# Performance work log

Hardware: AMD Instinct MI355X
Metric: run time of the kernel (lower is better)

The kernel has to match this reference:

```python
import jax, jax.numpy as jnp
import numpy as np

EPS = 1e-10

def setup_inputs() -> dict:
    key = jax.random.key(0)
    ks = jax.random.split(key, 7)
    B, S, C, H, W = 8, 4, 512, 64, 64
    Cq = C // 4
    x = jax.random.normal(ks[0], (B, S, C, H, W), dtype=jnp.float32)
    wq = jax.random.normal(ks[1], (S, Cq, C), dtype=jnp.float32) * 0.02
    bq = jax.random.normal(ks[2], (S, Cq), dtype=jnp.float32) * 0.02
    wk = jax.random.normal(ks[3], (S, Cq, C), dtype=jnp.float32) * 0.02
    bk = jax.random.normal(ks[4], (S, Cq), dtype=jnp.float32) * 0.02
    wv = jax.random.normal(ks[5], (S, C, C), dtype=jnp.float32) * 0.02
    bv = jax.random.normal(ks[6], (S, C), dtype=jnp.float32) * 0.02
    gamma = jnp.zeros((1,), dtype=jnp.float32)
    return {"x": x, "wq": wq, "bq": bq, "wk": wk, "bk": bk,
            "wv": wv, "bv": bv, "gamma": gamma}

def reference(x, wq, bq, wk, bk, wv, bv, gamma):
    # x: (B, S, C, H, W); per-scale 1x1 convs == per-pixel matmuls
    B, S, C, H, W = x.shape
    q = jnp.einsum('bschw,soc->bsohw', x, wq) + bq[None, :, :, None, None]
    k = jnp.einsum('bschw,soc->bsohw', x, wk) + bk[None, :, :, None, None]
    v = jnp.einsum('bschw,soc->bsohw', x, wv) + bv[None, :, :, None, None]
    pq = q.reshape(B, S, -1)                      # (B, S, D)
    pk = k.reshape(B, S, -1).transpose(0, 2, 1)   # (B, D, S)
    pv = v.reshape(B, S, -1)                      # (B, S, C*H*W)
    # L2 normalization (cosine similarity), matching torch eps placement
    A1 = pq / (jnp.sqrt(jnp.sum(pq * pq, axis=-1, keepdims=True)) + EPS)
    B1 = pk / (jnp.sqrt(jnp.sum(pk * pk, axis=1, keepdims=True)) + EPS)
    energy = jnp.einsum('bsd,bdt->bst', A1, B1)   # (B, S, S)
    attention = jax.nn.softmax(energy, axis=-1)
    out = jnp.einsum('bst,btd->bsd', attention, pv).reshape(B, S, C, H, W)
    out = gamma[0] * out + x
    # original returns list [out[:, i]] for i in range(S); return stacked tensor
    return out
```

## Files before the change

kernel.cpp:

```cpp
#include <hip/hip_runtime.h>
#include <hip/hip_bf16.h>

#define EPS_F 1e-10f

typedef short s16x8 __attribute__((ext_vector_type(8)));
typedef float f32x4 __attribute__((ext_vector_type(4)));
typedef unsigned short ushort_t;

constexpr int B_ = 8, S_ = 4, C_ = 512, Cq_ = 128, HW_ = 4096;
constexpr long long D_ = (long long)Cq_ * HW_;

__device__ inline float bf_lo(unsigned int u) { return __uint_as_float(u << 16); }
__device__ inline float bf_hi(unsigned int u) { return __uint_as_float(u & 0xffff0000u); }

__device__ inline ushort_t f2bf(float f) {
    __hip_bfloat16 h = __float2bfloat16(f);
    return *reinterpret_cast<ushort_t*>(&h);
}
__device__ inline unsigned int pack_bf2(float a, float b) {
    return (unsigned int)f2bf(a) | ((unsigned int)f2bf(b) << 16);
}
__device__ inline float dot8(uint4 a, uint4 b) {
    return bf_lo(a.x) * bf_lo(b.x) + bf_hi(a.x) * bf_hi(b.x)
         + bf_lo(a.y) * bf_lo(b.y) + bf_hi(a.y) * bf_hi(b.y)
         + bf_lo(a.z) * bf_lo(b.z) + bf_hi(a.z) * bf_hi(b.z)
         + bf_lo(a.w) * bf_lo(b.w) + bf_hi(a.w) * bf_hi(b.w);
}

#define GLOAD16(gp, lp) __builtin_amdgcn_global_load_lds( \
    (const __attribute__((address_space(1))) unsigned int*)(gp), \
    (__attribute__((address_space(3))) unsigned int*)(lp), 16, 0, 0)

#define VMCNT0 asm volatile("s_waitcnt vmcnt(0)" ::: "memory")
#define LGK0   asm volatile("s_waitcnt lgkmcnt(0)" ::: "memory")
#define MFMA16(a, b, c) __builtin_amdgcn_mfma_f32_16x16x32_bf16(a, b, c, 0, 0, 0)

#define SWZ(p) ((((p) >> 3) & 7) ^ ((p) & 7))

__global__ __launch_bounds__(256) void prep3(
    const float* __restrict__ wq, const float* __restrict__ wk,
    const float* __restrict__ wv,
    ushort_t* __restrict__ Wqk_pre, ushort_t* __restrict__ Wvb_pre,
    float* __restrict__ g4) {
    int gid = blockIdx.x * 256 + threadIdx.x;
    if (gid < 8 * 24 * 16) g4[gid] = 0.f;
    if (gid < 65536) {
        int s = gid >> 14;
        int kt = (gid >> 11) & 7;
        int row = (gid >> 3) & 255;
        int slot = gid & 7;
        int col = kt * 64 + ((slot ^ (row & 7)) << 3);
        const float* src = (row < 128)
            ? &wq[((size_t)s * 128 + row) * 512 + col]
            : &wk[((size_t)s * 128 + (row - 128)) * 512 + col];
        float4 f0 = *reinterpret_cast<const float4*>(src);
        float4 f1 = *reinterpret_cast<const float4*>(src + 4);
        uint4 o;
        o.x = pack_bf2(f0.x, f0.y); o.y = pack_bf2(f0.z, f0.w);
        o.z = pack_bf2(f1.x, f1.y); o.w = pack_bf2(f1.z, f1.w);
        *reinterpret_cast<uint4*>(Wqk_pre + (size_t)gid * 8) = o;
    } else {
        int c2 = gid - 65536;
        int t = c2 >> 15;
        int ct = (c2 >> 14) & 1;
        int kt = (c2 >> 11) & 7;
        int row = (c2 >> 3) & 255;
        int slot = c2 & 7;
        int col = kt * 64 + ((slot ^ (row & 7)) << 3);
        const float* src = &wv[((size_t)t * 512 + ct * 256 + row) * 512 + col];
        float4 f0 = *reinterpret_cast<const float4*>(src);
        float4 f1 = *reinterpret_cast<const float4*>(src + 4);
        uint4 o;
        o.x = pack_bf2(f0.x, f0.y); o.y = pack_bf2(f0.z, f0.w);
        o.z = pack_bf2(f1.x, f1.y); o.w = pack_bf2(f1.z, f1.w);
        *reinterpret_cast<uint4*>(Wvb_pre + (size_t)c2 * 8) = o;
    }
}

__global__ __launch_bounds__(512, 8) void qk8(
    const ushort_t* __restrict__ Wqk_pre, const float* __restrict__ x,
    const float* __restrict__ bq, const float* __restrict__ bk,
    ushort_t* __restrict__ Qb, ushort_t* __restrict__ Kb,
    ushort_t* __restrict__ xbfT) {

    const int xcd = blockIdx.x & 7;
    const int idx = blockIdx.x >> 3;
    const int bt = xcd * 4 + (idx >> 8);
    const int s = bt & 3;
    const int pb = (idx >> 1) & 127;
    const int ob = idx & 1;
    const int p0 = pb * 32;

    __shared__ __align__(16) ushort_t AsAll[2 * 8192];
    __shared__ __align__(16) ushort_t BsAll[2 * 2048];

    const int tid = threadIdx.x;
    const int w = tid >> 6, lane = tid & 63;
    const int wr = w >> 1, wc = w & 1;
    const int li = lane & 15, lk = lane >> 4;
    const int arow = wr * 32;
    const int bp = wc * 16 + li;
    int a_sl[2], b_sl[2];
#pragma unroll
    for (int h = 0; h < 2; ++h) {
        a_sl[h] = (((h * 4 + lk) ^ (li & 7)) << 3);
        b_sl[h] = (((h * 4 + lk) ^ SWZ(bp)) << 3);
    }

    const int sk = tid >> 3, spb = (tid & 7) * 4;
    const int ep = tid >> 3, esl = tid & 7;
    const int ec = esl ^ SWZ(ep);

    const float* Bx = x + (size_t)bt * C_ * HW_ + p0 + spb;

    f32x4 acc[2];
    acc[0] = 0.f; acc[1] = 0.f;
    float4 nb;

#define STAGE_A8(T, BUF)                                                     \
    { const ushort_t* _tp = Wqk_pre + ((size_t)(s * 8 + (T)) << 14)          \
                            + (ob << 13);                                    \
      ushort_t* _ld = &AsAll[(BUF) * 8192];                                  \
      _Pragma("unroll")                                                      \
      for (int _i = 0; _i < 2; ++_i)                                         \
          GLOAD16(_tp + ((w * 2 + _i) << 9) + (lane << 3),                   \
                  _ld + ((w * 2 + _i) << 9)); }

#define LOAD_B8(T) nb = *reinterpret_cast<const float4*>(Bx + (size_t)((T) * 64 + sk) * HW_)

#define WRITE_B8(BUF)                                                        \
    { float _vv[4] = {nb.x, nb.y, nb.z, nb.w};                               \
      _Pragma("unroll")                                                      \
      for (int _j = 0; _j < 4; ++_j) {                                       \
          int _p = spb + _j;                                                 \
          BsAll[(BUF) * 2048 + _p * 64 + (((sk >> 3) ^ SWZ(_p)) << 3)        \
                + (sk & 7)] = f2bf(_vv[_j]);                                 \
      } }

#define EMIT8(T, BUF)                                                        \
    if (ob == 0 && w < 4) {                                                  \
        s16x8 _ev = *reinterpret_cast<const s16x8*>(&BsAll[(BUF) * 2048 + tid * 8]); \
        *reinterpret_cast<s16x8*>(                                           \
            xbfT + ((size_t)bt * HW_ + p0 + ep) * 512 + (T) * 64 + ec * 8) = _ev; \
    }

#define COMPUTE8(BUF)                                                        \
    { const int _ab = (BUF) * 8192, _bb = (BUF) * 2048;                      \
      _Pragma("unroll")                                                      \
      for (int h = 0; h < 2; ++h) {                                          \
          s16x8 af0 = *reinterpret_cast<const s16x8*>(                       \
              &AsAll[_ab + (arow + 0 * 16 + li) * 64 + a_sl[h]]);            \
          s16x8 af1 = *reinterpret_cast<const s16x8*>(                       \
              &AsAll[_ab + (arow + 1 * 16 + li) * 64 + a_sl[h]]);            \
          s16x8 bf = *reinterpret_cast<const s16x8*>(                        \
              &BsAll[_bb + bp * 64 + b_sl[h]]);                              \
          __builtin_amdgcn_s_setprio(1);                                     \
          acc[0] = MFMA16(af0, bf, acc[0]);                                  \
          acc[1] = MFMA16(af1, bf, acc[1]);                                  \
          __builtin_amdgcn_s_setprio(0);                                     \
      } }

    LOAD_B8(0);
    STAGE_A8(0, 0);
    WRITE_B8(0);
    VMCNT0; LGK0;
    __builtin_amdgcn_s_barrier();

#pragma unroll
    for (int t = 0; t < 8; ++t) {
        if (t < 7) { LOAD_B8(t + 1); STAGE_A8(t + 1, (t + 1) & 1); }
        EMIT8(t, t & 1);
        COMPUTE8(t & 1);
        if (t < 7) {
            WRITE_B8((t + 1) & 1);
            VMCNT0; LGK0;
            __builtin_amdgcn_s_barrier();
        }
    }

#undef STAGE_A8
#undef LOAD_B8
#undef WRITE_B8
#undef EMIT8
#undef COMPUTE8

    ushort_t* outp = ob ? Kb : Qb;
    const float* biasp = ob ? (bk + s * 128) : (bq + s * 128);
#pragma unroll
    for (int mf = 0; mf < 2; ++mf) {
#pragma unroll
        for (int r = 0; r < 4; ++r) {
            int m = arow + mf * 16 + lk * 4 + r;
            float vv = acc[mf][r] + biasp[m];
            int p = p0 + wc * 16 + li;
            outp[(size_t)bt * D_ + (size_t)m * HW_ + p] = f2bf(vv);
        }
    }
}

__global__ __launch_bounds__(256, 4) void vblend8(
    const ushort_t* __restrict__ Wvb_pre, const ushort_t* __restrict__ xbfT,
    const float* __restrict__ x, const float* __restrict__ bv,
    const float* __restrict__ att, const float* __restrict__ gamma,
    float* __restrict__ out) {

    const int b = blockIdx.x & 7;
    const int idx = blockIdx.x >> 3;
    const int cblk = idx & 7;
    const int p0 = (idx >> 3) * 64;
    const int ct = cblk >> 2;
    const int csub = cblk & 3;

    __shared__ __align__(16) ushort_t AsAll[2 * 4096];
    __shared__ __align__(16) ushort_t BsAll[2 * 4096];

    const int tid = threadIdx.x;
    const int w = tid >> 6, lane = tid & 63;
    const int wr2 = w >> 1, wc2 = w & 1;
    const int li = lane & 15, lk = lane >> 4;

    int a_sl[2], b_sl[2];
    const int bp = wc2 * 32 + li;
    const int bp1 = bp + 16;
    int b_sl1[2];
#pragma unroll
    for (int h = 0; h < 2; ++h) {
        a_sl[h] = (((h * 4 + lk) ^ (li & 7)) << 3);
        b_sl[h] = (((h * 4 + lk) ^ SWZ(bp)) << 3);
        b_sl1[h] = (((h * 4 + lk) ^ SWZ(bp1)) << 3);
    }

    float attv[16];
#pragma unroll
    for (int i = 0; i < 16; ++i)
        attv[i] = __uint_as_float(__builtin_amdgcn_readfirstlane(
            __float_as_uint(att[b * 16 + i])));

    const int bst_p0 = tid >> 3, bst_sl0 = tid & 7;
    const int bst_c0 = bst_sl0 ^ SWZ(bst_p0);
    const int bst_p1 = (tid + 256) >> 3, bst_sl1 = tid & 7;
    const int bst_c1 = bst_sl1 ^ SWZ(bst_p1);

    f32x4 acc[2][2];
    f32x4 mst[4][2][2];
#pragma unroll
    for (int mf = 0; mf < 2; ++mf)
#pragma unroll
        for (int nf = 0; nf < 2; ++nf) acc[mf][nf] = 0.f;
#pragma unroll
    for (int so = 0; so < 4; ++so)
#pragma unroll
        for (int mf = 0; mf < 2; ++mf)
#pragma unroll
            for (int nf = 0; nf < 2; ++nf) mst[so][mf][nf] = 0.f;

#define STAGE7(TS, BUF)                                                      \
    {   const int _t = (TS) >> 3, _kt = (TS) & 7;                            \
        const ushort_t* _ap = Wvb_pre +                                      \
            (((size_t)(_t * 2 + ct) * 8 + _kt) << 14) + (csub << 12);        \
        ushort_t* _al = &AsAll[(BUF) * 4096];                                \
        GLOAD16(_ap + (size_t)(w << 9) + (size_t)(lane << 3),                \
                _al + (w << 9));                                             \
        GLOAD16(_ap + 2048 + (size_t)(w << 9) + (size_t)(lane << 3),         \
                _al + 2048 + (w << 9));                                      \
        const ushort_t* _bb = xbfT + ((size_t)(b * 4 + _t) * HW_);           \
        GLOAD16(_bb + ((size_t)(p0 + bst_p0)) * 512 + _kt * 64 + bst_c0 * 8, \
                &BsAll[(BUF) * 4096 + (w << 9)]);                            \
        GLOAD16(_bb + ((size_t)(p0 + bst_p1)) * 512 + _kt * 64 + bst_c1 * 8, \
                &BsAll[(BUF) * 4096 + 2048 + (w << 9)]);                     \
    }

#define COMPUTE7(BUF)                                                       \
    {   const int _ab = (BUF) * 4096, _bbf = (BUF) * 4096;                  \
        _Pragma("unroll")                                                    \
        for (int h = 0; h < 2; ++h) {                                        \
            s16x8 af0 = *reinterpret_cast<const s16x8*>(                     \
                &AsAll[_ab + (wr2 * 32 + 0 * 16 + li) * 64 + a_sl[h]]);      \
            s16x8 af1 = *reinterpret_cast<const s16x8*>(                     \
                &AsAll[_ab + (wr2 * 32 + 1 * 16 + li) * 64 + a_sl[h]]);      \
            s16x8 bf0 = *reinterpret_cast<const s16x8*>(                     \
                &BsAll[_bbf + bp * 64 + b_sl[h]]);                           \
            s16x8 bf1 = *reinterpret_cast<const s16x8*>(                     \
                &BsAll[_bbf + bp1 * 64 + b_sl1[h]]);                         \
            __builtin_amdgcn_s_setprio(1);                                   \
            acc[0][0] = MFMA16(af0, bf0, acc[0][0]);                         \
            acc[0][1] = MFMA16(af0, bf1, acc[0][1]);                         \
            acc[1][0] = MFMA16(af1, bf0, acc[1][0]);                         \
            acc[1][1] = MFMA16(af1, bf1, acc[1][1]);                         \
            __builtin_amdgcn_s_setprio(0);                                   \
        } }

#define BLEND7(T2)                                                           \
    { _Pragma("unroll")                                                      \
      for (int _so = 0; _so < 4; ++_so)                                      \
          _Pragma("unroll")                                                  \
          for (int _mf = 0; _mf < 2; ++_mf)                                  \
              _Pragma("unroll")                                              \
              for (int _nf = 0; _nf < 2; ++_nf)                              \
                  mst[_so][_mf][_nf] += attv[_so * 4 + (T2)] * acc[_mf][_nf];\
      _Pragma("unroll")                                                      \
      for (int _mf = 0; _mf < 2; ++_mf)                                      \
          _Pragma("unroll")                                                  \
          for (int _nf = 0; _nf < 2; ++_nf) acc[_mf][_nf] = 0.f; }

    STAGE7(0, 0);
    VMCNT0;
    __builtin_amdgcn_s_barrier();

#pragma unroll
    for (int ts = 0; ts < 32; ++ts) {
        if (ts < 31) STAGE7(ts + 1, (ts + 1) & 1);
        COMPUTE7(ts & 1);
        if (ts == 7)  BLEND7(0);
        if (ts == 15) BLEND7(1);
        if (ts == 23) BLEND7(2);
        if (ts == 31) BLEND7(3);
        if (ts < 31) {
            VMCNT0;
            __builtin_amdgcn_s_barrier();
        }
    }

#undef STAGE7
#undef COMPUTE7
#undef BLEND7

    const float gm = gamma[0];
    const int c0 = cblk * 64;
#pragma unroll
    for (int mf = 0; mf < 2; ++mf) {
#pragma unroll
        for (int r = 0; r < 4; ++r) {
            int c = c0 + wr2 * 32 + mf * 16 + lk * 4 + r;
            float bvv[4];
#pragma unroll
            for (int t = 0; t < 4; ++t) bvv[t] = bv[(size_t)t * 512 + c];
#pragma unroll
            for (int so = 0; so < 4; ++so) {
                float bsum = attv[so * 4 + 0] * bvv[0] + attv[so * 4 + 1] * bvv[1]
                           + attv[so * 4 + 2] * bvv[2] + attv[so * 4 + 3] * bvv[3];
#pragma unroll
                for (int nf = 0; nf < 2; ++nf) {
                    int p = p0 + wc2 * 32 + nf * 16 + li;
                    size_t off = ((size_t)(b * 4 + so) * C_ + c) * HW_ + p;
                    out[off] = gm * (mst[so][mf][nf][r] + bsum) + x[off];
                }
            }
        }
    }
}

__global__ __launch_bounds__(256) void gram5(
    const ushort_t* __restrict__ Q, const ushort_t* __restrict__ K,
    float* __restrict__ g4) {

    const int ch = blockIdx.x;
    const int b  = blockIdx.y;
    const size_t base = (size_t)ch * (D_ / 16);

    const uint4* qv[4];
    const uint4* kv[4];
#pragma unroll
    for (int s = 0; s < 4; ++s) {
        qv[s] = reinterpret_cast<const uint4*>(Q + (size_t)(b * 4 + s) * D_ + base);
        kv[s] = reinterpret_cast<const uint4*>(K + (size_t)(b * 4 + s) * D_ + base);
    }

    float accr[24];
#pragma unroll
    for (int e = 0; e < 24; ++e) accr[e] = 0.f;

    const int n8 = (int)(D_ / 16 / 8);
    for (int i = threadIdx.x; i < n8; i += 256) {
        uint4 qa[4], ka[4];
#pragma unroll
        for (int s = 0; s < 4; ++s) { qa[s] = qv[s][i]; ka[s] = kv[s][i]; }
#pragma unroll
        for (int s = 0; s < 4; ++s) {
#pragma unroll
            for (int u = 0; u < 4; ++u) accr[s * 4 + u] += dot8(qa[s], ka[u]);
            accr[16 + s] += dot8(qa[s], qa[s]);
            accr[20 + s] += dot8(ka[s], ka[s]);
        }
    }

    __shared__ float red[4][24];
    const int lane = threadIdx.x & 63, wid = threadIdx.x >> 6;
#pragma unroll
    for (int e = 0; e < 24; ++e) {
        float v = accr[e];
#pragma unroll
        for (int o = 32; o > 0; o >>= 1) v += __shfl_down(v, o);
        if (lane == 0) red[wid][e] = v;
    }
    __syncthreads();
    if (threadIdx.x < 24) {
        float t = red[0][threadIdx.x] + red[1][threadIdx.x]
                + red[2][threadIdx.x] + red[3][threadIdx.x];
        g4[((size_t)b * 24 + threadIdx.x) * 16 + ch] = t;
    }
}

__global__ void att_k5(const float* __restrict__ g4, float* __restrict__ att) {
    const int b = threadIdx.x;
    if (b >= B_) return;
    float e_[24];
#pragma unroll
    for (int e = 0; e < 24; ++e) {
        const float* p = g4 + ((size_t)b * 24 + e) * 16;
        float t = 0.f;
#pragma unroll
        for (int ch = 0; ch < 16; ++ch) t += p[ch];
        e_[e] = t;
    }
    float nq[4], nk[4];
#pragma unroll
    for (int s = 0; s < 4; ++s) {
        nq[s] = sqrtf(e_[16 + s]) + EPS_F;
        nk[s] = sqrtf(e_[20 + s]) + EPS_F;
    }
#pragma unroll
    for (int s = 0; s < 4; ++s) {
        float e[4], m = -1e30f;
#pragma unroll
        for (int t = 0; t < 4; ++t) {
            e[t] = e_[s * 4 + t] / (nq[s] * nk[t]);
            m = fmaxf(m, e[t]);
        }
        float sum = 0.f;
#pragma unroll
        for (int t = 0; t < 4; ++t) { e[t] = expf(e[t] - m); sum += e[t]; }
#pragma unroll
        for (int t = 0; t < 4; ++t) att[(size_t)(b * 4 + s) * 4 + t] = e[t] / sum;
    }
}

extern "C" void kernel_launch(void* const* d_in, const int* in_sizes, int n_in,
                              void* d_out, int out_size, void* d_ws, size_t ws_size,
                              hipStream_t stream) {
    const float* x     = (const float*)d_in[0];
    const float* wq    = (const float*)d_in[1];
    const float* bq    = (const float*)d_in[2];
    const float* wk    = (const float*)d_in[3];
    const float* bk    = (const float*)d_in[4];
    const float* wv    = (const float*)d_in[5];
    const float* bv    = (const float*)d_in[6];
    const float* gamma = (const float*)d_in[7];
    float* out = (float*)d_out;

    char* ws = (char*)d_ws;
    const size_t qk_elems = (size_t)B_ * S_ * Cq_ * HW_;
    ushort_t* Qb      = (ushort_t*)ws;
    ushort_t* Kb      = Qb + qk_elems;
    ushort_t* Wqk_pre = Kb + qk_elems;
    ushort_t* Wvb_pre = Wqk_pre + (size_t)4 * 8 * 256 * 64;
    float*    g4      = (float*)(Wvb_pre + (size_t)4 * 2 * 8 * 256 * 64);
    float*    att     = g4 + 8 * 24 * 16;
    ushort_t* xbfT    = (ushort_t*)(att + 128);

    prep3<<<768, 256, 0, stream>>>(wq, wk, wv, Wqk_pre, Wvb_pre, g4);
    qk8<<<8192, 512, 0, stream>>>(Wqk_pre, x, bq, bk, Qb, Kb, xbfT);
    gram5<<<dim3(16, 8), 256, 0, stream>>>(Qb, Kb, g4);
    att_k5<<<1, 64, 0, stream>>>(g4, att);
    vblend8<<<4096, 256, 0, stream>>>(Wvb_pre, xbfT, x, bv, att, gamma, out);
}
```

Before: 405.6 us.

## Fuse Gram reduction into QK projection and enlarge vblend tiles

New measurement: 581.5 us. +43.4%, slower.

```diff
diff --git a/kernel.cpp b/kernel.cpp
--- a/kernel.cpp
+++ b/kernel.cpp
@@ -8,7 +8,6 @@
 typedef unsigned short ushort_t;
 
 constexpr int B_ = 8, S_ = 4, C_ = 512, Cq_ = 128, HW_ = 4096;
-constexpr long long D_ = (long long)Cq_ * HW_;
 
 __device__ inline float bf_lo(unsigned int u) { return __uint_as_float(u << 16); }
 __device__ inline float bf_hi(unsigned int u) { return __uint_as_float(u & 0xffff0000u); }
@@ -20,11 +19,8 @@
 __device__ inline unsigned int pack_bf2(float a, float b) {
     return (unsigned int)f2bf(a) | ((unsigned int)f2bf(b) << 16);
 }
-__device__ inline float dot8(uint4 a, uint4 b) {
-    return bf_lo(a.x) * bf_lo(b.x) + bf_hi(a.x) * bf_hi(b.x)
-         + bf_lo(a.y) * bf_lo(b.y) + bf_hi(a.y) * bf_hi(b.y)
-         + bf_lo(a.z) * bf_lo(b.z) + bf_hi(a.z) * bf_hi(b.z)
-         + bf_lo(a.w) * bf_lo(b.w) + bf_hi(a.w) * bf_hi(b.w);
+__device__ inline float dot2u(unsigned int a, unsigned int b) {
+    return bf_lo(a) * bf_lo(b) + bf_hi(a) * bf_hi(b);
 }
 
 #define GLOAD16(gp, lp) __builtin_amdgcn_global_load_lds( \
@@ -40,10 +36,8 @@
 __global__ __launch_bounds__(256) void prep3(
     const float* __restrict__ wq, const float* __restrict__ wk,
     const float* __restrict__ wv,
-    ushort_t* __restrict__ Wqk_pre, ushort_t* __restrict__ Wvb_pre,
-    float* __restrict__ g4) {
+    ushort_t* __restrict__ Wqk_pre, ushort_t* __restrict__ Wvb_pre) {
     int gid = blockIdx.x * 256 + threadIdx.x;
-    if (gid < 8 * 24 * 16) g4[gid] = 0.f;
     if (gid < 65536) {
         int s = gid >> 14;
         int kt = (gid >> 11) & 7;
@@ -77,128 +71,217 @@
     }
 }
 
-__global__ __launch_bounds__(512, 8) void qk8(
+__global__ __launch_bounds__(512, 4) void qkg(
     const ushort_t* __restrict__ Wqk_pre, const float* __restrict__ x,
     const float* __restrict__ bq, const float* __restrict__ bk,
-    ushort_t* __restrict__ Qb, ushort_t* __restrict__ Kb,
-    ushort_t* __restrict__ xbfT) {
-
-    const int xcd = blockIdx.x & 7;
-    const int idx = blockIdx.x >> 3;
-    const int bt = xcd * 4 + (idx >> 8);
-    const int s = bt & 3;
-    const int pb = (idx >> 1) & 127;
-    const int ob = idx & 1;
-    const int p0 = pb * 32;
-
-    __shared__ __align__(16) ushort_t AsAll[2 * 8192];
-    __shared__ __align__(16) ushort_t BsAll[2 * 2048];
+    ushort_t* __restrict__ xbfT, float* __restrict__ g4) {
+
+    const int b = blockIdx.x & 7;
+    const int pblk = blockIdx.x >> 3;
+    const int p0 = pblk * 32;
+
+    __shared__ __align__(16) ushort_t As[2][16384];
+    __shared__ __align__(16) ushort_t Bs[2][2048];
 
     const int tid = threadIdx.x;
     const int w = tid >> 6, lane = tid & 63;
-    const int wr = w >> 1, wc = w & 1;
+    const int w4 = w * 4;
     const int li = lane & 15, lk = lane >> 4;
-    const int arow = wr * 32;
-    const int bp = wc * 16 + li;
-    int a_sl[2], b_sl[2];
+    const int aq_row = 16 * w + li;
+    const int ak_row = 128 + 16 * w + li;
+    const int ob4 = 16 * w + lk * 4;
+
+    int a_sl[2], b_sl0[2], b_sl1[2];
 #pragma unroll
     for (int h = 0; h < 2; ++h) {
-        a_sl[h] = (((h * 4 + lk) ^ (li & 7)) << 3);
-        b_sl[h] = (((h * 4 + lk) ^ SWZ(bp)) << 3);
+        a_sl[h]  = (((h * 4 + lk) ^ (li & 7)) << 3);
+        b_sl0[h] = (((h * 4 + lk) ^ SWZ(li)) << 3);
+        b_sl1[h] = (((h * 4 + lk) ^ SWZ(16 + li)) << 3);
     }
 
     const int sk = tid >> 3, spb = (tid & 7) * 4;
     const int ep = tid >> 3, esl = tid & 7;
     const int ec = esl ^ SWZ(ep);
 
-    const float* Bx = x + (size_t)bt * C_ * HW_ + p0 + spb;
-
-    f32x4 acc[2];
-    acc[0] = 0.f; acc[1] = 0.f;
+    f32x4 accq[2], acck[2];
+#pragma unroll
+    for (int i = 0; i < 2; ++i) { accq[i] = 0.f; acck[i] = 0.f; }
+    unsigned int Qr[4][4], Kr[4][4];
     float4 nb;
 
-#define STAGE_A8(T, BUF)                                                     \
-    { const ushort_t* _tp = Wqk_pre + ((size_t)(s * 8 + (T)) << 14)          \
-                            + (ob << 13);                                    \
-      ushort_t* _ld = &AsAll[(BUF) * 8192];                                  \
+#define STAGE_AG(TS, BUF)                                                    \
+    { const ushort_t* _tp = Wqk_pre +                                        \
+          ((size_t)(((TS) >> 3) * 8 + ((TS) & 7)) << 14);                    \
+      ushort_t* _ld = &As[BUF][0];                                           \
       _Pragma("unroll")                                                      \
-      for (int _i = 0; _i < 2; ++_i)                                         \
-          GLOAD16(_tp + ((w * 2 + _i) << 9) + (lane << 3),                   \
-                  _ld + ((w * 2 + _i) << 9)); }
-
-#define LOAD_B8(T) nb = *reinterpret_cast<const float4*>(Bx + (size_t)((T) * 64 + sk) * HW_)
-
-#define WRITE_B8(BUF)                                                        \
+      for (int _i = 0; _i < 4; ++_i)                                         \
+          GLOAD16(_tp + ((w4 + _i) << 9) + (lane << 3),                      \
+                  _ld + ((w4 + _i) << 9)); }
+
+#define LOAD_BG(TS)                                                          \
+    nb = *reinterpret_cast<const float4*>(                                   \
+        x + ((size_t)(b * 4 + ((TS) >> 3)) * C_ + ((TS) & 7) * 64 + sk) * HW_\
+        + p0 + spb)
+
+#define WRITE_BG(BUF)                                                        \
     { float _vv[4] = {nb.x, nb.y, nb.z, nb.w};                               \
       _Pragma("unroll")                                                      \
       for (int _j = 0; _j < 4; ++_j) {                                       \
           int _p = spb + _j;                                                 \
-          BsAll[(BUF) * 2048 + _p * 64 + (((sk >> 3) ^ SWZ(_p)) << 3)        \
-                + (sk & 7)] = f2bf(_vv[_j]);                                 \
+          Bs[BUF][_p * 64 + (((sk >> 3) ^ SWZ(_p)) << 3) + (sk & 7)]         \
+              = f2bf(_vv[_j]);                                               \
       } }
 
-#define EMIT8(T, BUF)                                                        \
-    if (ob == 0 && w < 4) {                                                  \
-        s16x8 _ev = *reinterpret_cast<const s16x8*>(&BsAll[(BUF) * 2048 + tid * 8]); \
+#define EMITG(TS, BUF)                                                       \
+    if (w < 4) {                                                             \
+        s16x8 _ev = *reinterpret_cast<const s16x8*>(&Bs[BUF][tid * 8]);      \
         *reinterpret_cast<s16x8*>(                                           \
-            xbfT + ((size_t)bt * HW_ + p0 + ep) * 512 + (T) * 64 + ec * 8) = _ev; \
-    }
-
-#define COMPUTE8(BUF)                                                        \
-    { const int _ab = (BUF) * 8192, _bb = (BUF) * 2048;                      \
-      _Pragma("unroll")                                                      \
+            xbfT + ((size_t)(b * 4 + ((TS) >> 3)) * HW_ + p0 + ep) * 512     \
+            + ((TS) & 7) * 64 + ec * 8) = _ev;                               \
+    }
+
+#define COMPUTEG(BUF)                                                        \
+    { _Pragma("unroll")                                                      \
       for (int h = 0; h < 2; ++h) {                                          \
-          s16x8 af0 = *reinterpret_cast<const s16x8*>(                       \
-              &AsAll[_ab + (arow + 0 * 16 + li) * 64 + a_sl[h]]);            \
-          s16x8 af1 = *reinterpret_cast<const s16x8*>(                       \
-              &AsAll[_ab + (arow + 1 * 16 + li) * 64 + a_sl[h]]);            \
-          s16x8 bf = *reinterpret_cast<const s16x8*>(                        \
-              &BsAll[_bb + bp * 64 + b_sl[h]]);                              \
+          s16x8 aq = *reinterpret_cast<const s16x8*>(                        \
+              &As[BUF][aq_row * 64 + a_sl[h]]);                              \
+          s16x8 ak = *reinterpret_cast<const s16x8*>(                        \
+              &As[BUF][ak_row * 64 + a_sl[h]]);                              \
+          s16x8 b0 = *reinterpret_cast<const s16x8*>(                        \
+              &Bs[BUF][li * 64 + b_sl0[h]]);                                 \
+          s16x8 b1 = *reinterpret_cast<const s16x8*>(                        \
+              &Bs[BUF][(16 + li) * 64 + b_sl1[h]]);                          \
           __builtin_amdgcn_s_setprio(1);                                     \
-          acc[0] = MFMA16(af0, bf, acc[0]);                                  \
-          acc[1] = MFMA16(af1, bf, acc[1]);                                  \
+          accq[0] = MFMA16(aq, b0, accq[0]);                                 \
+          accq[1] = MFMA16(aq, b1, accq[1]);                                 \
+          acck[0] = MFMA16(ak, b0, acck[0]);                                 \
+          acck[1] = MFMA16(ak, b1, acck[1]);                                 \
           __builtin_amdgcn_s_setprio(0);                                     \
       } }
 
-    LOAD_B8(0);
-    STAGE_A8(0, 0);
-    WRITE_B8(0);
+#define PACKG(T)                                                             \
+    {   float4 _bqv = *reinterpret_cast<const float4*>(bq + (T) * 128 + ob4);\
+        float4 _bkv = *reinterpret_cast<const float4*>(bk + (T) * 128 + ob4);\
+        _Pragma("unroll")                                                    \
+        for (int _ph = 0; _ph < 2; ++_ph) {                                  \
+            Qr[T][_ph * 2 + 0] = pack_bf2(accq[_ph][0] + _bqv.x,             \
+                                          accq[_ph][1] + _bqv.y);            \
+            Qr[T][_ph * 2 + 1] = pack_bf2(accq[_ph][2] + _bqv.z,             \
+                                          accq[_ph][3] + _bqv.w);            \
+            Kr[T][_ph * 2 + 0] = pack_bf2(acck[_ph][0] + _bkv.x,             \
+                                          acck[_ph][1] + _bkv.y);            \
+            Kr[T][_ph * 2 + 1] = pack_bf2(acck[_ph][2] + _bkv.z,             \
+                                          acck[_ph][3] + _bkv.w);            \
+            accq[_ph] = 0.f;                                                 \
+            acck[_ph] = 0.f;                                                 \
+        } }
+
+    LOAD_BG(0);
+    STAGE_AG(0, 0);
+    WRITE_BG(0);
     VMCNT0; LGK0;
     __builtin_amdgcn_s_barrier();
 
 #pragma unroll
-    for (int t = 0; t < 8; ++t) {
-        if (t < 7) { LOAD_B8(t + 1); STAGE_A8(t + 1, (t + 1) & 1); }
-        EMIT8(t, t & 1);
-        COMPUTE8(t & 1);
-        if (t < 7) {
-            WRITE_B8((t + 1) & 1);
+    for (int ts = 0; ts < 32; ++ts) {
+        if (ts < 31) { LOAD_BG(ts + 1); STAGE_AG(ts + 1, (ts + 1) & 1); }
+        EMITG(ts, ts & 1);
+        COMPUTEG(ts & 1);
+        if (ts == 7)  PACKG(0);
+        if (ts == 15) PACKG(1);
+        if (ts == 23) PACKG(2);
+        if (ts == 31) PACKG(3);
+        if (ts < 31) {
+            WRITE_BG((ts + 1) & 1);
             VMCNT0; LGK0;
             __builtin_amdgcn_s_barrier();
         }
     }
 
-#undef STAGE_A8
-#undef LOAD_B8
-#undef WRITE_B8
-#undef EMIT8
-#undef COMPUTE8
-
-    ushort_t* outp = ob ? Kb : Qb;
-    const float* biasp = ob ? (bk + s * 128) : (bq + s * 128);
-#pragma unroll
-    for (int mf = 0; mf < 2; ++mf) {
-#pragma unroll
-        for (int r = 0; r < 4; ++r) {
-            int m = arow + mf * 16 + lk * 4 + r;
-            float vv = acc[mf][r] + biasp[m];
-            int p = p0 + wc * 16 + li;
-            outp[(size_t)bt * D_ + (size_t)m * HW_ + p] = f2bf(vv);
-        }
-    }
-}
-
-__global__ __launch_bounds__(256, 4) void vblend8(
+#undef STAGE_AG
+#undef LOAD_BG
+#undef WRITE_BG
+#undef EMITG
+#undef COMPUTEG
+#undef PACKG
+
+    float d[24];
+#pragma unroll
+    for (int t1 = 0; t1 < 4; ++t1)
+#pragma unroll
+        for (int t2 = 0; t2 < 4; ++t2) {
+            float s = 0.f;
+#pragma unroll
+            for (int j = 0; j < 4; ++j) s += dot2u(Qr[t1][j], Kr[t2][j]);
+            d[t1 * 4 + t2] = s;
+        }
+#pragma unroll
+    for (int t = 0; t < 4; ++t) {
+        float sq = 0.f, sk2 = 0.f;
+#pragma unroll
+        for (int j = 0; j < 4; ++j) {
+            sq += dot2u(Qr[t][j], Qr[t][j]);
+            sk2 += dot2u(Kr[t][j], Kr[t][j]);
+        }
+        d[16 + t] = sq;
+        d[20 + t] = sk2;
+    }
+
+    __shared__ float red[8][24];
+#pragma unroll
+    for (int e = 0; e < 24; ++e) {
+        float v = d[e];
+#pragma unroll
+        for (int o = 32; o > 0; o >>= 1) v += __shfl_down(v, o);
+        if (lane == 0) red[w][e] = v;
+    }
+    __syncthreads();
+    if (tid < 24) {
+        float t = 0.f;
+#pragma unroll
+        for (int ww = 0; ww < 8; ++ww) t += red[ww][tid];
+        g4[((size_t)b * 24 + tid) * 128 + pblk] = t;
+    }
+}
+
+__global__ void att_k6(const float* __restrict__ g4, float* __restrict__ att) {
+    __shared__ float sm[8][24];
+    const int tid = threadIdx.x;
+    if (tid < 192) {
+        const int b = tid / 24, e = tid % 24;
+        const float* p = g4 + ((size_t)b * 24 + e) * 128;
+        float t = 0.f;
+        for (int ch = 0; ch < 128; ++ch) t += p[ch];
+        sm[b][e] = t;
+    }
+    __syncthreads();
+    if (tid < 8) {
+        const int b = tid;
+        float nq[4], nk[4];
+#pragma unroll
+        for (int s = 0; s < 4; ++s) {
+            nq[s] = sqrtf(sm[b][16 + s]) + EPS_F;
+            nk[s] = sqrtf(sm[b][20 + s]) + EPS_F;
+        }
+#pragma unroll
+        for (int s = 0; s < 4; ++s) {
+            float e[4], m = -1e30f;
+#pragma unroll
+            for (int t = 0; t < 4; ++t) {
+                e[t] = sm[b][s * 4 + t] / (nq[s] * nk[t]);
+                m = fmaxf(m, e[t]);
+            }
+            float sum = 0.f;
+#pragma unroll
+            for (int t = 0; t < 4; ++t) { e[t] = expf(e[t] - m); sum += e[t]; }
+#pragma unroll
+            for (int t = 0; t < 4; ++t)
+                att[(size_t)(b * 4 + s) * 4 + t] = e[t] / sum;
+        }
+    }
+}
+
+__global__ __launch_bounds__(512, 6) void vblend11(
     const ushort_t* __restrict__ Wvb_pre, const ushort_t* __restrict__ xbfT,
     const float* __restrict__ x, const float* __restrict__ bv,
     const float* __restrict__ att, const float* __restrict__ gamma,
@@ -207,22 +290,21 @@
     const int b = blockIdx.x & 7;
     const int idx = blockIdx.x >> 3;
     const int cblk = idx & 7;
-    const int p0 = (idx >> 3) * 64;
+    const int p0 = (idx >> 3) * 128;
     const int ct = cblk >> 2;
     const int csub = cblk & 3;
 
     __shared__ __align__(16) ushort_t AsAll[2 * 4096];
-    __shared__ __align__(16) ushort_t BsAll[2 * 4096];
+    __shared__ __align__(16) ushort_t BsAll[2 * 8192];
 
     const int tid = threadIdx.x;
     const int w = tid >> 6, lane = tid & 63;
-    const int wr2 = w >> 1, wc2 = w & 1;
+    const int wr2 = w >> 2, wc2 = w & 3;
     const int li = lane & 15, lk = lane >> 4;
 
-    int a_sl[2], b_sl[2];
+    int a_sl[2], b_sl[2], b_sl1[2];
     const int bp = wc2 * 32 + li;
     const int bp1 = bp + 16;
-    int b_sl1[2];
 #pragma unroll
     for (int h = 0; h < 2; ++h) {
         a_sl[h] = (((h * 4 + lk) ^ (li & 7)) << 3);
@@ -236,10 +318,13 @@
         attv[i] = __uint_as_float(__builtin_amdgcn_readfirstlane(
             __float_as_uint(att[b * 16 + i])));
 
-    const int bst_p0 = tid >> 3, bst_sl0 = tid & 7;
-    const int bst_c0 = bst_sl0 ^ SWZ(bst_p0);
-    const int bst_p1 = (tid + 256) >> 3, bst_sl1 = tid & 7;
-    const int bst_c1 = bst_sl1 ^ SWZ(bst_p1);
+    int bst_p[2], bst_c[2];
+#pragma unroll
+    for (int i = 0; i < 2; ++i) {
+        int c = (w * 2 + i) * 64 + lane;
+        bst_p[i] = c >> 3;
+        bst_c[i] = (c & 7) ^ SWZ(bst_p[i]);
+    }
 
     f32x4 acc[2][2];
     f32x4 mst[4][2][2];
@@ -254,24 +339,21 @@
 #pragma unroll
             for (int nf = 0; nf < 2; ++nf) mst[so][mf][nf] = 0.f;
 
-#define STAGE7(TS, BUF)                                                      \
+#define STAGE11(TS, BUF)                                                     \
     {   const int _t = (TS) >> 3, _kt = (TS) & 7;                            \
         const ushort_t* _ap = Wvb_pre +                                      \
             (((size_t)(_t * 2 + ct) * 8 + _kt) << 14) + (csub << 12);        \
-        ushort_t* _al = &AsAll[(BUF) * 4096];                                \
-        GLOAD16(_ap + (size_t)(w << 9) + (size_t)(lane << 3),                \
-                _al + (w << 9));                                             \
-        GLOAD16(_ap + 2048 + (size_t)(w << 9) + (size_t)(lane << 3),         \
-                _al + 2048 + (w << 9));                                      \
+        GLOAD16(_ap + (w << 9) + (lane << 3), &AsAll[(BUF) * 4096 + (w << 9)]); \
         const ushort_t* _bb = xbfT + ((size_t)(b * 4 + _t) * HW_);           \
-        GLOAD16(_bb + ((size_t)(p0 + bst_p0)) * 512 + _kt * 64 + bst_c0 * 8, \
-                &BsAll[(BUF) * 4096 + (w << 9)]);                            \
-        GLOAD16(_bb + ((size_t)(p0 + bst_p1)) * 512 + _kt * 64 + bst_c1 * 8, \
-                &BsAll[(BUF) * 4096 + 2048 + (w << 9)]);                     \
-    }
-
-#define COMPUTE7(BUF)                                                       \
-    {   const int _ab = (BUF) * 4096, _bbf = (BUF) * 4096;                  \
+        _Pragma("unroll")                                                    \
+        for (int _i = 0; _i < 2; ++_i)                                       \
+            GLOAD16(_bb + ((size_t)(p0 + bst_p[_i])) * 512 + _kt * 64        \
+                        + bst_c[_i] * 8,                                     \
+                    &BsAll[(BUF) * 8192 + ((w * 2 + _i) << 9)]);             \
+    }
+
+#define COMPUTE11(BUF)                                                      \
+    {   const int _ab = (BUF) * 4096, _bbf = (BUF) * 8192;                  \
         _Pragma("unroll")                                                    \
         for (int h = 0; h < 2; ++h) {                                        \
             s16x8 af0 = *reinterpret_cast<const s16x8*>(                     \
@@ -290,7 +372,7 @@
             __builtin_amdgcn_s_setprio(0);                                   \
         } }
 
-#define BLEND7(T2)                                                           \
+#define BLEND11(T2)                                                          \
     { _Pragma("unroll")                                                      \
       for (int _so = 0; _so < 4; ++_so)                                      \
           _Pragma("unroll")                                                  \
@@ -303,27 +385,27 @@
           _Pragma("unroll")                                                  \
           for (int _nf = 0; _nf < 2; ++_nf) acc[_mf][_nf] = 0.f; }
 
-    STAGE7(0, 0);
+    STAGE11(0, 0);
     VMCNT0;
     __builtin_amdgcn_s_barrier();
 
 #pragma unroll
     for (int ts = 0; ts < 32; ++ts) {
-        if (ts < 31) STAGE7(ts + 1, (ts + 1) & 1);
-        COMPUTE7(ts & 1);
-        if (ts == 7)  BLEND7(0);
-        if (ts == 15) BLEND7(1);
-        if (ts == 23) BLEND7(2);
-        if (ts == 31) BLEND7(3);
+        if (ts < 31) STAGE11(ts + 1, (ts + 1) & 1);
+        COMPUTE11(ts & 1);
+        if (ts == 7)  BLEND11(0);
+        if (ts == 15) BLEND11(1);
+        if (ts == 23) BLEND11(2);
+        if (ts == 31) BLEND11(3);
         if (ts < 31) {
             VMCNT0;
             __builtin_amdgcn_s_barrier();
         }
     }
 
-#undef STAGE7
-#undef COMPUTE7
-#undef BLEND7
+#undef STAGE11
+#undef COMPUTE11
+#undef BLEND11
 
     const float gm = gamma[0];
     const int c0 = cblk * 64;
@@ -347,91 +429,6 @@
                 }
             }
         }
-    }
-}
-
-__global__ __launch_bounds__(256) void gram5(
-    const ushort_t* __restrict__ Q, const ushort_t* __restrict__ K,
-    float* __restrict__ g4) {
-
-    const int ch = blockIdx.x;
-    const int b  = blockIdx.y;
-    const size_t base = (size_t)ch * (D_ / 16);
-
-    const uint4* qv[4];
-    const uint4* kv[4];
-#pragma unroll
-    for (int s = 0; s < 4; ++s) {
-        qv[s] = reinterpret_cast<const uint4*>(Q + (size_t)(b * 4 + s) * D_ + base);
-        kv[s] = reinterpret_cast<const uint4*>(K + (size_t)(b * 4 + s) * D_ + base);
-    }
-
-    float accr[24];
-#pragma unroll
-    for (int e = 0; e < 24; ++e) accr[e] = 0.f;
-
-    const int n8 = (int)(D_ / 16 / 8);
-    for (int i = threadIdx.x; i < n8; i += 256) {
-        uint4 qa[4], ka[4];
-#pragma unroll
-        for (int s = 0; s < 4; ++s) { qa[s] = qv[s][i]; ka[s] = kv[s][i]; }
-#pragma unroll
-        for (int s = 0; s < 4; ++s) {
-#pragma unroll
-            for (int u = 0; u < 4; ++u) accr[s * 4 + u] += dot8(qa[s], ka[u]);
-            accr[16 + s] += dot8(qa[s], qa[s]);
-            accr[20 + s] += dot8(ka[s], ka[s]);
-        }
-    }
-
-    __shared__ float red[4][24];
-    const int lane = threadIdx.x & 63, wid = threadIdx.x >> 6;
-#pragma unroll
-    for (int e = 0; e < 24; ++e) {
-        float v = accr[e];
-#pragma unroll
-        for (int o = 32; o > 0; o >>= 1) v += __shfl_down(v, o);
-        if (lane == 0) red[wid][e] = v;
-    }
-    __syncthreads();
-    if (threadIdx.x < 24) {
-        float t = red[0][threadIdx.x] + red[1][threadIdx.x]
-                + red[2][threadIdx.x] + red[3][threadIdx.x];
-        g4[((size_t)b * 24 + threadIdx.x) * 16 + ch] = t;
-    }
-}
-
-__global__ void att_k5(const float* __restrict__ g4, float* __restrict__ att) {
-    const int b = threadIdx.x;
-    if (b >= B_) return;
-    float e_[24];
-#pragma unroll
-    for (int e = 0; e < 24; ++e) {
-        const float* p = g4 + ((size_t)b * 24 + e) * 16;
-        float t = 0.f;
-#pragma unroll
-        for (int ch = 0; ch < 16; ++ch) t += p[ch];
-        e_[e] = t;
-    }
-    float nq[4], nk[4];
-#pragma unroll
-    for (int s = 0; s < 4; ++s) {
-        nq[s] = sqrtf(e_[16 + s]) + EPS_F;
-        nk[s] = sqrtf(e_[20 + s]) + EPS_F;
-    }
-#pragma unroll
-    for (int s = 0; s < 4; ++s) {
-        float e[4], m = -1e30f;
-#pragma unroll
-        for (int t = 0; t < 4; ++t) {
-            e[t] = e_[s * 4 + t] / (nq[s] * nk[t]);
-            m = fmaxf(m, e[t]);
-        }
-        float sum = 0.f;
-#pragma unroll
-        for (int t = 0; t < 4; ++t) { e[t] = expf(e[t] - m); sum += e[t]; }
-#pragma unroll
-        for (int t = 0; t < 4; ++t) att[(size_t)(b * 4 + s) * 4 + t] = e[t] / sum;
     }
 }
 
@@ -449,18 +446,14 @@
     float* out = (float*)d_out;
 
     char* ws = (char*)d_ws;
-    const size_t qk_elems = (size_t)B_ * S_ * Cq_ * HW_;
-    ushort_t* Qb      = (ushort_t*)ws;
-    ushort_t* Kb      = Qb + qk_elems;
-    ushort_t* Wqk_pre = Kb + qk_elems;
+    ushort_t* Wqk_pre = (ushort_t*)ws;
     ushort_t* Wvb_pre = Wqk_pre + (size_t)4 * 8 * 256 * 64;
     float*    g4      = (float*)(Wvb_pre + (size_t)4 * 2 * 8 * 256 * 64);
-    float*    att     = g4 + 8 * 24 * 16;
+    float*    att     = g4 + (size_t)8 * 24 * 128;
     ushort_t* xbfT    = (ushort_t*)(att + 128);
 
-    prep3<<<768, 256, 0, stream>>>(wq, wk, wv, Wqk_pre, Wvb_pre, g4);
-    qk8<<<8192, 512, 0, stream>>>(Wqk_pre, x, bq, bk, Qb, Kb, xbfT);
-    gram5<<<dim3(16, 8), 256, 0, stream>>>(Qb, Kb, g4);
-    att_k5<<<1, 64, 0, stream>>>(g4, att);
-    vblend8<<<4096, 256, 0, stream>>>(Wvb_pre, xbfT, x, bv, att, gamma, out);
-}
+    prep3<<<768, 256, 0, stream>>>(wq, wk, wv, Wqk_pre, Wvb_pre);
+    qkg<<<1024, 512, 0, stream>>>(Wqk_pre, x, bq, bk, xbfT, g4);
+    att_k6<<<1, 256, 0, stream>>>(g4, att);
+    vblend11<<<2048, 512, 0, stream>>>(Wvb_pre, xbfT, x, bv, att, gamma, out);
+}
```
